# Performance work log

Hardware: AMD Instinct MI355X
Metric: run time of the kernel (lower is better)

## Reference

```python
import jax, jax.numpy as jnp
import numpy as np

N, D = 16384, 128

def setup_inputs() -> dict:
    key = jax.random.key(0)
    k1, k2 = jax.random.split(key)
    x = jax.random.normal(k1, (N, D), dtype=jnp.float32)
    adj = jax.random.randint(k2, (N, N), 0, 2, dtype=jnp.int32)
    return {"x": x, "adj": adj}

def reference(x, adj):
    # out[i] = x[i] + sum_{j: adj[i,j]==1} x[j]  ==  (adj + I) @ x
    a = adj.astype(x.dtype)
    return x + jnp.matmul(a, x)  # [N, D]
```

## Files before the change

### kernel.cpp

```cpp
#include <hip/hip_runtime.h>
#include <hip/hip_bf16.h>

#define GN 16384
#define GD 128
#define KSPLIT 4
#define KBLK (GN / KSPLIT)
#define CHUNK_K 128
#define NCHUNK (KBLK / CHUNK_K)
#define CHUNK_SHORTS (GD * CHUNK_K)
#define OUT_ELEMS (GN * GD)

typedef __attribute__((ext_vector_type(8))) short short8;
typedef __attribute__((ext_vector_type(4))) float floatx4;
typedef __attribute__((ext_vector_type(4))) int intx4;

static __device__ __forceinline__ unsigned short f32_to_bf16(float f) {
  unsigned u = __builtin_bit_cast(unsigned, f);
  unsigned r = u + 0x7FFFu + ((u >> 16) & 1u);
  return (unsigned short)(r >> 16);
}

__global__ __launch_bounds__(256) void prep_kernel(const float* __restrict__ x,
                                                   unsigned short* __restrict__ xT) {
  __shared__ unsigned short t[GD][66];
  const int tid = threadIdx.x;
  const int j0 = blockIdx.x * 64;
  for (int i = tid; i < 64 * GD; i += 256) {
    int j = i >> 7, d = i & (GD - 1);
    t[d][j] = f32_to_bf16(x[(size_t)(j0 + j) * GD + d]);
  }
  __syncthreads();
  for (int i = tid; i < GD * 32; i += 256) {
    int d = i >> 5, jp = i & 31;
    unsigned lo = t[d][2 * jp], hi = t[d][2 * jp + 1];
    *reinterpret_cast<unsigned*>(xT + (size_t)d * GN + j0 + 2 * jp) = lo | (hi << 16);
  }
}

__global__ __launch_bounds__(256, 2) void gemm_kernel(const int* __restrict__ adj,
                                                      const unsigned short* __restrict__ xT,
                                                      float* __restrict__ partials) {
  __shared__ unsigned short bbuf[2][CHUNK_SHORTS];
  const int tid = threadIdx.x;
  const int wave = tid >> 6;
  const int lane = tid & 63;
  const int q = lane >> 4;
  const int m = lane & 15;
  const int rbase = blockIdx.x * 128 + wave * 32;
  const int kbase = blockIdx.y * KBLK;

  const unsigned short* gptr[8];
  unsigned short* lptr[8];
#pragma unroll
  for (int p = 0; p < 8; ++p) {
    int s = tid + 256 * p;
    int n = s >> 4;
    int gsrc = (s & 15) ^ (n & 15);
    gptr[p] = xT + (size_t)n * GN + kbase + gsrc * 8;
    lptr[p] = &bbuf[0][0] + (size_t)s * 8;
  }

#define STAGE(bufsel, koff)                                                              \
  do {                                                                                   \
    _Pragma("unroll") for (int p = 0; p < 8; ++p) {                                      \
      __builtin_amdgcn_global_load_lds(                                                  \
          (const __attribute__((address_space(1))) unsigned int*)(gptr[p] + (koff)),     \
          (__attribute__((address_space(3))) unsigned int*)(lptr[p] +                    \
                                                           (bufsel) * CHUNK_SHORTS),     \
          16, 0, 0);                                                                     \
    }                                                                                    \
  } while (0)

  const int* a0 = adj + (size_t)(rbase + m) * GN + kbase + q * 8;
  const int* a1 = adj + (size_t)(rbase + 16 + m) * GN + kbase + q * 8;

  floatx4 acc[2][8];
#pragma unroll
  for (int t = 0; t < 2; ++t)
#pragma unroll
    for (int c = 0; c < 8; ++c) acc[t][c] = (floatx4){0.f, 0.f, 0.f, 0.f};

  STAGE(0, 0);

  int buf = 0;
  for (int c = 0; c < NCHUNK; ++c) {
    __syncthreads();
    if (c < NCHUNK - 1) STAGE(buf ^ 1, (c + 1) * CHUNK_K);

#pragma unroll
    for (int kk = 0; kk < 4; ++kk) {
      const int koff = c * CHUNK_K + kk * 32;
      intx4 r0 = __builtin_nontemporal_load((const intx4*)(a0 + koff));
      intx4 r1 = __builtin_nontemporal_load((const intx4*)(a0 + koff + 4));
      intx4 r2 = __builtin_nontemporal_load((const intx4*)(a1 + koff));
      intx4 r3 = __builtin_nontemporal_load((const intx4*)(a1 + koff + 4));

      short8 bf[8];
      const unsigned short* bb = &bbuf[buf][0];
      const int gsw = ((4 * kk + q) ^ m) * 8;
#pragma unroll
      for (int cc = 0; cc < 8; ++cc)
        bf[cc] = *(const short8*)(bb + (cc * 16 + m) * CHUNK_K + gsw);

      intx4 p0, p1;
      p0.x = (r0.x | (r0.y << 16)) * 0x3F80;
      p0.y = (r0.z | (r0.w << 16)) * 0x3F80;
      p0.z = (r1.x | (r1.y << 16)) * 0x3F80;
      p0.w = (r1.z | (r1.w << 16)) * 0x3F80;
      p1.x = (r2.x | (r2.y << 16)) * 0x3F80;
      p1.y = (r2.z | (r2.w << 16)) * 0x3F80;
      p1.z = (r3.x | (r3.y << 16)) * 0x3F80;
      p1.w = (r3.z | (r3.w << 16)) * 0x3F80;
      short8 af0 = __builtin_bit_cast(short8, p0);
      short8 af1 = __builtin_bit_cast(short8, p1);

#pragma unroll
      for (int cc = 0; cc < 8; ++cc) {
        acc[0][cc] = __builtin_amdgcn_mfma_f32_16x16x32_bf16(af0, bf[cc], acc[0][cc], 0, 0, 0);
        acc[1][cc] = __builtin_amdgcn_mfma_f32_16x16x32_bf16(af1, bf[cc], acc[1][cc], 0, 0, 0);
      }
    }
    buf ^= 1;
  }

  float* pp = partials + (size_t)blockIdx.y * OUT_ELEMS + (size_t)rbase * GD;
#pragma unroll
  for (int t = 0; t < 2; ++t)
#pragma unroll
    for (int cc = 0; cc < 8; ++cc)
#pragma unroll
      for (int r = 0; r < 4; ++r) {
        int row = t * 16 + q * 4 + r;
        int col = cc * 16 + m;
        pp[(size_t)row * GD + col] = acc[t][cc][r];
      }
}

__global__ __launch_bounds__(256) void reduce_kernel(const float* __restrict__ x,
                                                     const float* __restrict__ partials,
                                                     float* __restrict__ out) {
  size_t i = ((size_t)blockIdx.x * 256 + threadIdx.x) * 4;
  floatx4 v = *(const floatx4*)(x + i);
  v += *(const floatx4*)(partials + 0 * (size_t)OUT_ELEMS + i);
  v += *(const floatx4*)(partials + 1 * (size_t)OUT_ELEMS + i);
  v += *(const floatx4*)(partials + 2 * (size_t)OUT_ELEMS + i);
  v += *(const floatx4*)(partials + 3 * (size_t)OUT_ELEMS + i);
  *(floatx4*)(out + i) = v;
}

extern "C" void kernel_launch(void* const* d_in, const int* in_sizes, int n_in,
                              void* d_out, int out_size, void* d_ws, size_t ws_size,
                              hipStream_t stream) {
  const float* x = (const float*)d_in[0];
  const int* adj = (const int*)d_in[1];
  float* out = (float*)d_out;
  unsigned short* xT = (unsigned short*)d_ws;
  float* partials = (float*)((char*)d_ws + (size_t)GN * GD * 2);

  prep_kernel<<<GN / 64, 256, 0, stream>>>(x, xT);
  gemm_kernel<<<dim3(GN / 128, KSPLIT), 256, 0, stream>>>(adj, xT, partials);
  reduce_kernel<<<OUT_ELEMS / 4 / 256, 256, 0, stream>>>(x, partials, out);
}
```

Measured before the change: 1.428 ms.

## Drop LDS staging; single-wave blocks load B fragments directly with register prefetch

The GEMM kernel switches from 256-thread blocks that share a double-buffered LDS copy of the xT chunk to one-wave blocks. Each wave loads its bf16 B fragments straight from global memory into registers and prefetches the next k-step's A and B into registers. This removes LDS staging and block-wide barriers, but the four waves that previously shared each B tile now each read it from global memory/L2 separately. The kernel is bound by streaming the int32 adjacency matrix, so the extra B traffic may or may not matter.

```diff
diff --git a/kernel.cpp b/kernel.cpp
--- a/kernel.cpp
+++ b/kernel.cpp
@@ -5,9 +5,6 @@
 #define GD 128
 #define KSPLIT 4
 #define KBLK (GN / KSPLIT)
-#define CHUNK_K 128
-#define NCHUNK (KBLK / CHUNK_K)
-#define CHUNK_SHORTS (GD * CHUNK_K)
 #define OUT_ELEMS (GN * GD)
 
 typedef __attribute__((ext_vector_type(8))) short short8;
@@ -37,42 +34,20 @@
   }
 }
 
-__global__ __launch_bounds__(256, 2) void gemm_kernel(const int* __restrict__ adj,
-                                                      const unsigned short* __restrict__ xT,
-                                                      float* __restrict__ partials) {
-  __shared__ unsigned short bbuf[2][CHUNK_SHORTS];
-  const int tid = threadIdx.x;
-  const int wave = tid >> 6;
-  const int lane = tid & 63;
+__global__ __launch_bounds__(64, 2) void gemm_kernel(const int* __restrict__ adj,
+                                                     const unsigned short* __restrict__ xT,
+                                                     float* __restrict__ partials) {
+  const int lane = threadIdx.x;
   const int q = lane >> 4;
   const int m = lane & 15;
-  const int rbase = blockIdx.x * 128 + wave * 32;
-  const int kbase = blockIdx.y * KBLK;
-
-  const unsigned short* gptr[8];
-  unsigned short* lptr[8];
-#pragma unroll
-  for (int p = 0; p < 8; ++p) {
-    int s = tid + 256 * p;
-    int n = s >> 4;
-    int gsrc = (s & 15) ^ (n & 15);
-    gptr[p] = xT + (size_t)n * GN + kbase + gsrc * 8;
-    lptr[p] = &bbuf[0][0] + (size_t)s * 8;
-  }
-
-#define STAGE(bufsel, koff)                                                              \
-  do {                                                                                   \
-    _Pragma("unroll") for (int p = 0; p < 8; ++p) {                                      \
-      __builtin_amdgcn_global_load_lds(                                                  \
-          (const __attribute__((address_space(1))) unsigned int*)(gptr[p] + (koff)),     \
-          (__attribute__((address_space(3))) unsigned int*)(lptr[p] +                    \
-                                                           (bufsel) * CHUNK_SHORTS),     \
-          16, 0, 0);                                                                     \
-    }                                                                                    \
-  } while (0)
+  const int wid = blockIdx.x;
+  const int rbase = (wid >> 2) * 32;
+  const int ks = wid & 3;
+  const int kbase = ks * KBLK;
 
   const int* a0 = adj + (size_t)(rbase + m) * GN + kbase + q * 8;
-  const int* a1 = adj + (size_t)(rbase + 16 + m) * GN + kbase + q * 8;
+  const int* a1 = a0 + (size_t)16 * GN;
+  const unsigned short* b0 = xT + (size_t)m * GN + kbase + q * 8;
 
   floatx4 acc[2][8];
 #pragma unroll
@@ -80,59 +55,60 @@
 #pragma unroll
     for (int c = 0; c < 8; ++c) acc[t][c] = (floatx4){0.f, 0.f, 0.f, 0.f};
 
-  STAGE(0, 0);
+  intx4 r0 = __builtin_nontemporal_load((const intx4*)(a0));
+  intx4 r1 = __builtin_nontemporal_load((const intx4*)(a0 + 4));
+  intx4 r2 = __builtin_nontemporal_load((const intx4*)(a1));
+  intx4 r3 = __builtin_nontemporal_load((const intx4*)(a1 + 4));
+  short8 bf[8];
+#pragma unroll
+  for (int c = 0; c < 8; ++c)
+    bf[c] = *(const short8*)(b0 + (size_t)c * 16 * GN);
 
-  int buf = 0;
-  for (int c = 0; c < NCHUNK; ++c) {
-    __syncthreads();
-    if (c < NCHUNK - 1) STAGE(buf ^ 1, (c + 1) * CHUNK_K);
+  for (int k = 0; k < KBLK; k += 32) {
+    const int kn = (k + 32) & (KBLK - 1);
+
+    intx4 s0 = __builtin_nontemporal_load((const intx4*)(a0 + kn));
+    intx4 s1 = __builtin_nontemporal_load((const intx4*)(a0 + kn + 4));
+    intx4 s2 = __builtin_nontemporal_load((const intx4*)(a1 + kn));
+    intx4 s3 = __builtin_nontemporal_load((const intx4*)(a1 + kn + 4));
+    short8 nbf[8];
+#pragma unroll
+    for (int c = 0; c < 8; ++c)
+      nbf[c] = *(const short8*)(b0 + (size_t)c * 16 * GN + kn);
+
+    intx4 p0, p1;
+    p0.x = (r0.x | (r0.y << 16)) * 0x3F80;
+    p0.y = (r0.z | (r0.w << 16)) * 0x3F80;
+    p0.z = (r1.x | (r1.y << 16)) * 0x3F80;
+    p0.w = (r1.z | (r1.w << 16)) * 0x3F80;
+    p1.x = (r2.x | (r2.y << 16)) * 0x3F80;
+    p1.y = (r2.z | (r2.w << 16)) * 0x3F80;
+    p1.z = (r3.x | (r3.y << 16)) * 0x3F80;
+    p1.w = (r3.z | (r3.w << 16)) * 0x3F80;
+    short8 af0 = __builtin_bit_cast(short8, p0);
+    short8 af1 = __builtin_bit_cast(short8, p1);
 
 #pragma unroll
-    for (int kk = 0; kk < 4; ++kk) {
-      const int koff = c * CHUNK_K + kk * 32;
-      intx4 r0 = __builtin_nontemporal_load((const intx4*)(a0 + koff));
-      intx4 r1 = __builtin_nontemporal_load((const intx4*)(a0 + koff + 4));
-      intx4 r2 = __builtin_nontemporal_load((const intx4*)(a1 + koff));
-      intx4 r3 = __builtin_nontemporal_load((const intx4*)(a1 + koff + 4));
+    for (int c = 0; c < 8; ++c) {
+      acc[0][c] = __builtin_amdgcn_mfma_f32_16x16x32_bf16(af0, bf[c], acc[0][c], 0, 0, 0);
+      acc[1][c] = __builtin_amdgcn_mfma_f32_16x16x32_bf16(af1, bf[c], acc[1][c], 0, 0, 0);
+    }
 
-      short8 bf[8];
-      const unsigned short* bb = &bbuf[buf][0];
-      const int gsw = ((4 * kk + q) ^ m) * 8;
+    r0 = s0; r1 = s1; r2 = s2; r3 = s3;
 #pragma unroll
-      for (int cc = 0; cc < 8; ++cc)
-        bf[cc] = *(const short8*)(bb + (cc * 16 + m) * CHUNK_K + gsw);
-
-      intx4 p0, p1;
-      p0.x = (r0.x | (r0.y << 16)) * 0x3F80;
-      p0.y = (r0.z | (r0.w << 16)) * 0x3F80;
-      p0.z = (r1.x | (r1.y << 16)) * 0x3F80;
-      p0.w = (r1.z | (r1.w << 16)) * 0x3F80;
-      p1.x = (r2.x | (r2.y << 16)) * 0x3F80;
-      p1.y = (r2.z | (r2.w << 16)) * 0x3F80;
-      p1.z = (r3.x | (r3.y << 16)) * 0x3F80;
-      p1.w = (r3.z | (r3.w << 16)) * 0x3F80;
-      short8 af0 = __builtin_bit_cast(short8, p0);
-      short8 af1 = __builtin_bit_cast(short8, p1);
-
-#pragma unroll
-      for (int cc = 0; cc < 8; ++cc) {
-        acc[0][cc] = __builtin_amdgcn_mfma_f32_16x16x32_bf16(af0, bf[cc], acc[0][cc], 0, 0, 0);
-        acc[1][cc] = __builtin_amdgcn_mfma_f32_16x16x32_bf16(af1, bf[cc], acc[1][cc], 0, 0, 0);
-      }
-    }
-    buf ^= 1;
+    for (int c = 0; c < 8; ++c) bf[c] = nbf[c];
   }
 
-  float* pp = partials + (size_t)blockIdx.y * OUT_ELEMS + (size_t)rbase * GD;
+  float* pp = partials + (size_t)ks * OUT_ELEMS + (size_t)rbase * GD;
 #pragma unroll
   for (int t = 0; t < 2; ++t)
 #pragma unroll
-    for (int cc = 0; cc < 8; ++cc)
+    for (int c = 0; c < 8; ++c)
 #pragma unroll
       for (int r = 0; r < 4; ++r) {
         int row = t * 16 + q * 4 + r;
-        int col = cc * 16 + m;
-        pp[(size_t)row * GD + col] = acc[t][cc][r];
+        int col = c * 16 + m;
+        pp[(size_t)row * GD + col] = acc[t][c][r];
       }
 }
 
@@ -158,6 +134,6 @@
   float* partials = (float*)((char*)d_ws + (size_t)GN * GD * 2);
 
   prep_kernel<<<GN / 64, 256, 0, stream>>>(x, xT);
-  gemm_kernel<<<dim3(GN / 128, KSPLIT), 256, 0, stream>>>(adj, xT, partials);
+  gemm_kernel<<<(GN / 32) * KSPLIT, 64, 0, stream>>>(adj, xT, partials);
   reduce_kernel<<<OUT_ELEMS / 4 / 256, 256, 0, stream>>>(x, partials, out);
 }
```

Measured after the change: 1.555 ms. 1.09x slower.
